# Optimization experiments

Hardware: AMD Instinct MI355X
Metric: run time of the kernel (lower is better)

The kernel has to match this reference:

```python
import jax, jax.numpy as jnp
import numpy as np

B, S, E, F = 8, 1024, 1024, 4096
EPS = 1e-12

def _layer_norm(x, gamma, beta):
    mu = jnp.mean(x, axis=-1, keepdims=True)
    var = jnp.mean(jnp.square(x - mu), axis=-1, keepdims=True)
    return (x - mu) / jnp.sqrt(var + EPS) * gamma + beta

def setup_inputs() -> dict:
    key = jax.random.key(0)
    ks = jax.random.split(key, 16)
    sE = 1.0 / np.sqrt(E)
    sF = 1.0 / np.sqrt(F)
    return {
        'hidden_states': jax.random.normal(ks[0], (B, S, E), jnp.float32),
        'Wq': jax.random.normal(ks[1], (E, E), jnp.float32) * sE,
        'bq': jnp.zeros((E,), jnp.float32),
        'Wk': jax.random.normal(ks[2], (E, E), jnp.float32) * sE,
        'bk': jnp.zeros((E,), jnp.float32),
        'Wv': jax.random.normal(ks[3], (E, E), jnp.float32) * sE,
        'bv': jnp.zeros((E,), jnp.float32),
        'Wd': jax.random.normal(ks[4], (E, E), jnp.float32) * sE,
        'bd': jnp.zeros((E,), jnp.float32),
        'g1': jnp.ones((E,), jnp.float32),
        'b1': jnp.zeros((E,), jnp.float32),
        'Wi': jax.random.normal(ks[5], (E, F), jnp.float32) * sE,
        'bi': jnp.zeros((F,), jnp.float32),
        'Wo': jax.random.normal(ks[6], (F, E), jnp.float32) * sF,
        'bo': jnp.zeros((E,), jnp.float32),
        'g2': jnp.ones((E,), jnp.float32),
        'b2': jnp.zeros((E,), jnp.float32),
    }

def reference(hidden_states, Wq, bq, Wk, bk, Wv, bv, Wd, bd, g1, b1, Wi, bi, Wo, bo, g2, b2):
    x = hidden_states
    q = x @ Wq + bq                     # [B,S,E]
    k = x @ Wk + bk
    v = x @ Wv + bv
    scores = jnp.einsum('bqe,bke->bqk', q, k) / jnp.sqrt(jnp.float32(E))
    attn_w = jax.nn.softmax(scores, axis=-1)
    attn_out = jnp.einsum('bqk,bke->bqe', attn_w, v)
    # add_norm 1 (dropout = identity in eval)
    h1 = _layer_norm(attn_out @ Wd + bd + x, g1, b1)
    ff = jax.nn.gelu(h1 @ Wi + bi, approximate=False)   # forward_act
    # NOTE: original code's second add_norm uses forward_act (pre out_dense),
    # applying out_dense inside add_norm -> LN(out_dense(ff) + h1)
    out = _layer_norm(ff @ Wo + bo + h1, g2, b2)
    return out
```

## Files before the change

### kernel.cpp

```cpp
#include <hip/hip_runtime.h>
#include <math.h>


typedef __bf16 bf16;
typedef __attribute__((ext_vector_type(8))) __bf16 bf16x8;
typedef __attribute__((ext_vector_type(4))) __bf16 bf16x4;
typedef __attribute__((ext_vector_type(4))) float f32x4;

#define BM 128
#define BN 128
#define BK 64
#define SCS 140

__device__ __forceinline__ void async_cp16(const bf16* g, bf16* l) {
    __builtin_amdgcn_global_load_lds((__attribute__((address_space(1))) void*)(g),
                                     (__attribute__((address_space(3))) void*)(l),
                                     16, 0, 0);
}

__device__ __forceinline__ float gelu_fast(float x) {
    float u = x * x;
    float y = 1.5957691216f * x * fmaf(0.044715f, u, 1.0f);
    float e = __expf(-y);
    return x * __builtin_amdgcn_rcpf(1.0f + e);
}

__device__ __forceinline__ float load_dual(const void* p, long long i, int f32) {
    return f32 ? ((const float*)p)[i] : (float)((const bf16*)p)[i];
}


__global__ void diag_init(const void* x, int* dflag)
{
    const int t = threadIdx.x;
    const bf16* xb = (const bf16*)x;
    float a = (float)xb[2 * t];
    float b = (float)xb[2 * t + 1];
    auto wild = [](float v) -> bool {
        float af = fabsf(v);
        return !(af <= 3.0e38f) || af > 1.0e3f || (v != 0.0f && af < 1.0e-8f);
    };
    unsigned long long ba = __ballot(wild(a));
    unsigned long long bb = __ballot(wild(b));
    if (t == 0) *dflag = (__popcll(ba) + __popcll(bb) > 16) ? 1 : 0;
}

__global__ void sentinel_small(float* out) { out[0] = 2048.0f; }


__global__ __launch_bounds__(256)
void convert_vec4(const void* src, bf16* dst, long long n4, const int* dflag)
{
    const int f32 = *dflag;
    long long i = (long long)blockIdx.x * 256 + threadIdx.x;
    if (i >= n4) return;
    bf16x4 o;
    if (f32) {
        f32x4 v = ((const f32x4*)src)[i];
        #pragma unroll
        for (int j = 0; j < 4; j++) o[j] = (bf16)v[j];
    } else {
        o = ((const bf16x4*)src)[i];
    }
    ((bf16x4*)dst)[i] = o;
}

struct SmallPtrs { const void* p[10]; };

__global__ __launch_bounds__(256)
void convert_small(SmallPtrs sp, bf16* dst, const int* dflag)
{
    const int f32 = *dflag;
    const int idx = blockIdx.x * 256 + threadIdx.x;
    if (idx >= 13312) return;
    const int seg = idx >> 10;
    float v;
    if (seg < 9) v = load_dual(sp.p[seg], idx & 1023, f32);
    else         v = load_dual(sp.p[9], idx - 9216, f32);
    dst[idx] = (bf16)v;
}

__global__ __launch_bounds__(256)
void transpose_dual(const void* in, bf16* out, int R, int C, const int* dflag)
{
    __shared__ bf16 tile[32][33];
    const int f32 = *dflag;
    const int c0 = blockIdx.x * 32, r0 = blockIdx.y * 32;
    const int tx = threadIdx.x, ty = threadIdx.y;
    #pragma unroll
    for (int i = 0; i < 32; i += 8)
        tile[ty + i][tx] = (bf16)load_dual(in, (long long)(r0 + ty + i) * C + (c0 + tx), f32);
    __syncthreads();
    #pragma unroll
    for (int i = 0; i < 32; i += 8)
        out[(long long)(c0 + ty + i) * R + (r0 + tx)] = tile[tx][ty + i];
}

__global__ __launch_bounds__(256)
void transpose_b(const bf16* __restrict__ in, bf16* __restrict__ out, int R, int C)
{
    __shared__ bf16 tile[32][33];
    const long long z = (long long)blockIdx.z * (long long)R * C;
    const int c0 = blockIdx.x * 32, r0 = blockIdx.y * 32;
    const int tx = threadIdx.x, ty = threadIdx.y;
    #pragma unroll
    for (int i = 0; i < 32; i += 8)
        tile[ty + i][tx] = in[z + (long long)(r0 + ty + i) * C + (c0 + tx)];
    __syncthreads();
    #pragma unroll
    for (int i = 0; i < 32; i += 8)
        out[z + (long long)(c0 + ty + i) * R + (r0 + tx)] = tile[tx][ty + i];
}

template<int ACT, int HAS_BIAS, int HAS_RES, int OUT_F32>
__global__ __launch_bounds__(512)
void gemm_bt(const bf16* __restrict__ A, const bf16* __restrict__ Bt,
             const bf16* __restrict__ bias, const bf16* __restrict__ res,
             void* __restrict__ Cout, int M, int N, int K, float scale,
             long long bsA, long long bsB, long long bsC, long long bsBias)
{
    __shared__ __align__(16) char smem[65536];
    float* sC = (float*)smem;

    const int tid  = threadIdx.x;
    const int lane = tid & 63;
    const int wave = tid >> 6;
    const int pw   = wave & 3;
    const int wm   = pw >> 1;
    const int wn   = pw & 1;
    const bool producer = (wave >= 4);
    const int m0   = blockIdx.y * BM;
    const int n0   = blockIdx.x * BN;
    const long long zA = (long long)blockIdx.z * bsA;
    const long long zB = (long long)blockIdx.z * bsB;
    const long long zC = (long long)blockIdx.z * bsC;
    const bf16* biasz = HAS_BIAS ? (bias + (long long)blockIdx.z * bsBias) : nullptr;
    const int nIter = K >> 6;

    f32x4 acc[4][4];
    const bf16* gA[4]; const bf16* gB[4]; int lo[4];

    if (producer) {
        #pragma unroll
        for (int j = 0; j < 4; j++) {
            const int ci  = j * 256 + pw * 64 + lane;
            const int row = ci >> 3;
            const int c8  = ((ci & 7) ^ (row & 7)) * 8;
            gA[j] = A + zA + (long long)(m0 + row) * K + c8;
            gB[j] = Bt + zB + (long long)(n0 + row) * K + c8;
            lo[j] = (j * 256 + pw * 64) * 8;
        }
        bf16* dA = (bf16*)smem;
        bf16* dB = (bf16*)(smem + 16384);
        #pragma unroll
        for (int j = 0; j < 4; j++) {
            async_cp16(gA[j], dA + lo[j]);
            async_cp16(gB[j], dB + lo[j]);
            gA[j] += BK; gB[j] += BK;
        }
    } else {
        const f32x4 zf = {0.f, 0.f, 0.f, 0.f};
        #pragma unroll
        for (int i = 0; i < 4; i++)
            #pragma unroll
            for (int j = 0; j < 4; j++) acc[i][j] = zf;
    }
    __syncthreads();

    const int fr   = lane & 15;
    const int x0   = (lane >> 4) ^ (fr & 7);
    const int arow = wm * 64 + fr;
    const int brow = wn * 64 + fr;

    for (int kt = 0; kt < nIter; ++kt) {
        if (producer) {
            if (kt + 1 < nIter) {
                const int bo = ((kt + 1) & 1) ? 32768 : 0;
                bf16* dA = (bf16*)(smem + bo);
                bf16* dB = (bf16*)(smem + bo + 16384);
                #pragma unroll
                for (int j = 0; j < 4; j++) {
                    async_cp16(gA[j], dA + lo[j]);
                    async_cp16(gB[j], dB + lo[j]);
                    gA[j] += BK; gB[j] += BK;
                }
            }
        } else {
            const int bo = (kt & 1) ? 32768 : 0;
            const bf16* sAk = (const bf16*)(smem + bo);
            const bf16* sBk = (const bf16*)(smem + bo + 16384);
            #pragma unroll
            for (int s = 0; s < 2; s++) {
                const int xo = (x0 ^ (s << 2)) * 8;
                bf16x8 afr[4], bfr[4];
                #pragma unroll
                for (int mi = 0; mi < 4; mi++) afr[mi] = *(const bf16x8*)(sAk + (arow + mi * 16) * 64 + xo);
                #pragma unroll
                for (int ni = 0; ni < 4; ni++) bfr[ni] = *(const bf16x8*)(sBk + (brow + ni * 16) * 64 + xo);
                #pragma unroll
                for (int mi = 0; mi < 4; mi++)
                    #pragma unroll
                    for (int ni = 0; ni < 4; ni++)
                        acc[mi][ni] = __builtin_amdgcn_mfma_f32_16x16x32_bf16(afr[mi], bfr[ni], acc[mi][ni], 0, 0, 0);
            }
        }
        __syncthreads();
    }

    const int q4 = lane >> 4;
    for (int h = 0; h < 2; h++) {
        __syncthreads();
        if (!producer && wm == h) {
            #pragma unroll
            for (int mi = 0; mi < 4; mi++)
                #pragma unroll
                for (int r = 0; r < 4; r++) {
                    const int lr = mi * 16 + q4 * 4 + r;
                    #pragma unroll
                    for (int ni = 0; ni < 4; ni++)
                        sC[lr * SCS + wn * 64 + ni * 16 + fr] = acc[mi][ni][r];
                }
        }
        __syncthreads();
        const int lr = tid >> 3;
        const int cb = (tid & 7) * 16;
        const long long grow  = m0 + h * 64 + lr;
        const long long gbase = zC + grow * (long long)N + (n0 + cb);
        const float* srow = sC + lr * SCS + cb;
        #pragma unroll
        for (int g = 0; g < 2; g++) {
            f32x4 v0 = *(const f32x4*)(srow + g * 8);
            f32x4 v1 = *(const f32x4*)(srow + g * 8 + 4);
            float vv[8] = {v0[0], v0[1], v0[2], v0[3], v1[0], v1[1], v1[2], v1[3]};
            if constexpr (HAS_BIAS) {
                bf16x8 bb = *(const bf16x8*)(biasz + n0 + cb + g * 8);
                #pragma unroll
                for (int j = 0; j < 8; j++) vv[j] = vv[j] * scale + (float)bb[j];
            } else {
                #pragma unroll
                for (int j = 0; j < 8; j++) vv[j] *= scale;
            }
            if constexpr (ACT == 1) {
                #pragma unroll
                for (int j = 0; j < 8; j++) vv[j] = gelu_fast(vv[j]);
            }
            if constexpr (HAS_RES) {
                bf16x8 rr = *(const bf16x8*)(res + gbase + g * 8);
                #pragma unroll
                for (int j = 0; j < 8; j++) vv[j] += (float)rr[j];
            }
            if constexpr (OUT_F32) {
                f32x4 o0 = {vv[0], vv[1], vv[2], vv[3]};
                f32x4 o1 = {vv[4], vv[5], vv[6], vv[7]};
                *(f32x4*)((float*)Cout + gbase + g * 8)     = o0;
                *(f32x4*)((float*)Cout + gbase + g * 8 + 4) = o1;
            } else {
                bf16x8 o;
                #pragma unroll
                for (int j = 0; j < 8; j++) o[j] = (bf16)vv[j];
                *(bf16x8*)((bf16*)Cout + gbase + g * 8) = o;
            }
        }
    }
}

template<int ACT, int HAS_BIAS, int HAS_RES, int OUT_F32, int SPLITK>
__global__ __launch_bounds__(512, 2)
void gemm256(const bf16* __restrict__ A, const bf16* __restrict__ Bt,
             const bf16* __restrict__ bias, const bf16* __restrict__ res,
             void* __restrict__ Cout, void* __restrict__ Cout2,
             int M, int N, int K, int ldk, float scale,
             long long bsB, long long bsC, long long bsBias)
{
    __shared__ __align__(16) char smem[131072];

    const int tid  = threadIdx.x;
    const int lane = tid & 63;
    const int wave = tid >> 6;
    const int wm   = wave >> 2;
    const int wn   = wave & 3;

    const int gx  = N >> 8;
    const int nwg = gx * (M >> 8);
    int wg = blockIdx.x;
    {
        const int q = nwg >> 3, r = nwg & 7;
        const int xcd = wg & 7, lid = wg >> 3;
        wg = (xcd < r ? xcd * (q + 1) : r * (q + 1) + (xcd - r) * q) + lid;
    }
    const int bx = wg % gx, by = wg / gx;
    const int m0 = by << 8, n0 = bx << 8;
    const int zi = blockIdx.y;

    const bf16* Ab = A  + (SPLITK ? (long long)zi * K : 0);
    const bf16* Bb = Bt + (SPLITK ? (long long)zi * K : (long long)zi * bsB);
    const bool  bon = HAS_BIAS && (!SPLITK || zi == 0);
    const bool  ron = HAS_RES  && (!SPLITK || zi == 0);
    const bf16* biasz = HAS_BIAS ? (bias + (SPLITK ? 0 : (long long)zi * bsBias)) : nullptr;
    const long long coff = SPLITK ? 0 : (long long)zi * bsC;
    char* const Cb = (char*)((SPLITK && zi) ? Cout2 : Cout);

    const int rg0 = wave * 16 + (lane >> 3);
    const int cg0 = (lane & 7) ^ (lane >> 3);
    const bf16* aSrc[2]; const bf16* bSrc[2];
    #pragma unroll
    for (int h = 0; h < 2; h++) {
        aSrc[h] = Ab + (long long)(m0 + h * 128 + rg0) * ldk + cg0 * 8;
        bSrc[h] = Bb + (long long)(n0 + h * 128 + rg0) * ldk + cg0 * 8;
    }
    const int sq8 = 8 * ldk;

    const int fr = lane & 15, chk = lane >> 4;
    unsigned aAddr[4], bAddr[4];
    {
        const unsigned sm3 = (unsigned)(size_t)(__attribute__((address_space(3))) char*)smem;
        #pragma unroll
        for (int cb = 0; cb < 2; cb++)
            #pragma unroll
            for (int kk = 0; kk < 2; kk++) {
                const unsigned slot = (unsigned)(((kk * 4 + chk) ^ (fr & 7)) * 16);
                aAddr[cb * 2 + kk] = sm3 + cb * 65536 + wm * 16384
                                   + fr * 128 + slot;
                bAddr[cb * 2 + kk] = sm3 + cb * 65536 + 32768 + (wn >> 1) * 16384
                                   + ((wn & 1) * 64 + fr) * 128 + slot;
            }
    }

#define DSR(d, b, imm) \
    asm volatile("ds_read_b128 %0, %1 offset:%c2" : "=v"(d) : "v"(b), "i"(imm))
#define RDA4(set, cb, q) do { \
    DSR(set[0], aAddr[(cb) * 2 + 0], (q) * 4096); \
    DSR(set[1], aAddr[(cb) * 2 + 1], (q) * 4096); \
    DSR(set[2], aAddr[(cb) * 2 + 0], (q) * 4096 + 2048); \
    DSR(set[3], aAddr[(cb) * 2 + 1], (q) * 4096 + 2048); \
} while (0)
#define RDB8(cb) do { \
    DSR(bv[0], bAddr[(cb) * 2 + 0], 0);    DSR(bv[1], bAddr[(cb) * 2 + 1], 0); \
    DSR(bv[2], bAddr[(cb) * 2 + 0], 2048); DSR(bv[3], bAddr[(cb) * 2 + 1], 2048); \
    DSR(bv[4], bAddr[(cb) * 2 + 0], 4096); DSR(bv[5], bAddr[(cb) * 2 + 1], 4096); \
    DSR(bv[6], bAddr[(cb) * 2 + 0], 6144); DSR(bv[7], bAddr[(cb) * 2 + 1], 6144); \
} while (0)
#define STG(buf, mat, h, t) do { \
    bf16* _d = (bf16*)(smem + (buf) * 65536 + (mat) * 32768 + (h) * 16384 + wave * 2048); \
    const bf16* _s = ((mat) ? bSrc[h] : aSrc[h]) + (t) * 64; \
    async_cp16(_s, _d); \
    async_cp16(_s + sq8, _d + 512); \
} while (0)
#define IF_STG(c, buf, mat, h, t) do { if (c) STG(buf, mat, h, t); } while (0)
#define BARR __builtin_amdgcn_s_barrier()
#define SB0  __builtin_amdgcn_sched_barrier(0)
#define LGKM0 asm volatile("s_waitcnt lgkmcnt(0)")
#define VM_WAIT(c) do { \
    if (c) asm volatile("s_waitcnt vmcnt(4)"); \
    else   asm volatile("s_waitcnt vmcnt(0)"); \
} while (0)
#define MMA(q, ASET) do { \
    __builtin_amdgcn_s_setprio(1); \
    _Pragma("unroll") \
    for (int _j = 0; _j < 4; _j++) { \
        acc[(q) * 2 + 0][_j] = __builtin_amdgcn_mfma_f32_16x16x32_bf16(ASET[0], bv[_j * 2 + 0], acc[(q) * 2 + 0][_j], 0, 0, 0); \
        acc[(q) * 2 + 1][_j] = __builtin_amdgcn_mfma_f32_16x16x32_bf16(ASET[2], bv[_j * 2 + 0], acc[(q) * 2 + 1][_j], 0, 0, 0); \
    } \
    _Pragma("unroll") \
    for (int _j = 0; _j < 4; _j++) { \
        acc[(q) * 2 + 0][_j] = __builtin_amdgcn_mfma_f32_16x16x32_bf16(ASET[1], bv[_j * 2 + 1], acc[(q) * 2 + 0][_j], 0, 0, 0); \
        acc[(q) * 2 + 1][_j] = __builtin_amdgcn_mfma_f32_16x16x32_bf16(ASET[3], bv[_j * 2 + 1], acc[(q) * 2 + 1][_j], 0, 0, 0); \
    } \
    __builtin_amdgcn_s_setprio(0); \
} while (0)

    const int NT = K >> 6, NI = NT >> 1;

    STG(0, 0, 0, 0); STG(0, 0, 1, 0); STG(0, 1, 0, 0); STG(0, 1, 1, 0);
    STG(1, 1, 0, 1); STG(1, 1, 1, 1);

    f32x4 acc[8][4];
    {
        const f32x4 zf = {0.f, 0.f, 0.f, 0.f};
        #pragma unroll
        for (int i = 0; i < 8; i++)
            #pragma unroll
            for (int j = 0; j < 4; j++) acc[i][j] = zf;
    }
    bf16x8 avA[4], avB[4], bv[8];

    asm volatile("s_waitcnt vmcnt(4)");
    BARR;

    for (int it = 0; it < NI; ++it) {
        const int o = 2 * it + 1, e2 = 2 * it + 2, o2 = 2 * it + 3;
        const bool se = e2 < NT, so = o2 < NT;
        RDB8(0);
        RDA4(avA, 0, 0);
        STG(1, 0, 0, o);
        BARR; LGKM0; SB0;
        RDA4(avB, 0, 1); SB0;
        MMA(0, avA);
        BARR;
        STG(1, 0, 1, o);
        BARR; LGKM0; SB0;
        RDA4(avA, 0, 2); SB0;
        MMA(1, avB);
        BARR;
        IF_STG(se, 0, 1, 0, e2);
        BARR; LGKM0; SB0;
        RDA4(avB, 0, 3); SB0;
        MMA(2, avA);
        BARR;
        IF_STG(se, 0, 1, 1, e2);
        BARR; LGKM0; SB0;
        MMA(3, avB); SB0;
        VM_WAIT(se);
        BARR;
        RDB8(1);
        RDA4(avA, 1, 0);
        IF_STG(se, 0, 0, 0, e2);
        BARR; LGKM0; SB0;
        RDA4(avB, 1, 1); SB0;
        MMA(0, avA);
        BARR;
        IF_STG(se, 0, 0, 1, e2);
        BARR; LGKM0; SB0;
        RDA4(avA, 1, 2); SB0;
        MMA(1, avB);
        BARR;
        IF_STG(so, 1, 1, 0, o2);
        BARR; LGKM0; SB0;
        RDA4(avB, 1, 3); SB0;
        MMA(2, avA);
        BARR;
        IF_STG(so, 1, 1, 1, o2);
        BARR; LGKM0; SB0;
        MMA(3, avB); SB0;
        VM_WAIT(so);
        BARR;
    }
#undef MMA
#undef VM_WAIT
#undef LGKM0
#undef SB0
#undef BARR
#undef IF_STG
#undef STG
#undef RDB8
#undef RDA4
#undef DSR

    float* sC = (float*)smem;
    const int q4 = lane >> 4;
    const int lr = tid >> 3;
    const int c0 = (tid & 7) * 4;
    const long long Nll = N;
    #pragma unroll
    for (int p = 0; p < 4; p++) {
        __syncthreads();
        if (wm == (p >> 1)) {
            #pragma unroll
            for (int i = 0; i < 4; i++) {
                const int fi = (p & 1) * 4 + i;
                #pragma unroll
                for (int r = 0; r < 4; r++) {
                    const int row = i * 16 + q4 * 4 + r;
                    #pragma unroll
                    for (int j = 0; j < 4; j++)
                        sC[row * 260 + wn * 64 + j * 16 + fr] = acc[fi][j][r];
                }
            }
        }
        __syncthreads();
        const long long grow = m0 + p * 64 + lr;
        const long long gb = grow * Nll + n0;
        const float* srow = sC + lr * 260;
        #pragma unroll
        for (int g = 0; g < 8; g++) {
            const int col = c0 + g * 32;
            f32x4 v = *(const f32x4*)(srow + col);
            float vv[4] = {v[0], v[1], v[2], v[3]};
            if (bon) {
                bf16x4 bb = *(const bf16x4*)(biasz + n0 + col);
                #pragma unroll
                for (int j = 0; j < 4; j++) vv[j] = vv[j] * scale + (float)bb[j];
            } else {
                #pragma unroll
                for (int j = 0; j < 4; j++) vv[j] *= scale;
            }
            if constexpr (ACT == 1) {
                #pragma unroll
                for (int j = 0; j < 4; j++) vv[j] = gelu_fast(vv[j]);
            }
            if (ron) {
                bf16x4 rr = *(const bf16x4*)(res + gb + col);
                #pragma unroll
                for (int j = 0; j < 4; j++) vv[j] += (float)rr[j];
            }
            if constexpr (OUT_F32) {
                f32x4 o4 = {vv[0], vv[1], vv[2], vv[3]};
                *(f32x4*)((float*)Cb + coff + gb + col) = o4;
            } else {
                bf16x4 o4;
                #pragma unroll
                for (int j = 0; j < 4; j++) o4[j] = (bf16)vv[j];
                *(bf16x4*)((bf16*)Cb + coff + gb + col) = o4;
            }
        }
    }
}

template<int ACT, int HAS_BIAS, int HAS_RES, int OUT_F32, int SPLITK>
__global__ __launch_bounds__(512, 4)
void gemm128d(const bf16* __restrict__ A, const bf16* __restrict__ Bt,
              const bf16* __restrict__ bias, const bf16* __restrict__ res,
              void* __restrict__ Cout, void* __restrict__ Cout2,
              int M, int N, int K, int ldk, float scale,
              long long bsA, long long bsB, long long bsC, long long bsBias)
{
    __shared__ __align__(16) char smem[65536];

    const int tid  = threadIdx.x;
    const int lane = tid & 63;
    const int wave = tid >> 6;
    const int wm   = wave >> 2;
    const int wn   = wave & 3;

    const int gx  = N >> 7;
    const int nwg = gx * (M >> 7);
    int wg = blockIdx.x;
    {
        const int q = nwg >> 3, r = nwg & 7;
        const int xcd = wg & 7, lid = wg >> 3;
        wg = (xcd < r ? xcd * (q + 1) : r * (q + 1) + (xcd - r) * q) + lid;
    }
    const int bx = wg % gx, by = wg / gx;
    const int m0 = by << 7, n0 = bx << 7;
    const int zi = blockIdx.y;

    const bf16* Ab = A  + (SPLITK ? (long long)zi * K : (long long)zi * bsA);
    const bf16* Bb = Bt + (SPLITK ? (long long)zi * K : (long long)zi * bsB);
    const bool  bon = HAS_BIAS && (!SPLITK || zi == 0);
    const bool  ron = HAS_RES  && (!SPLITK || zi == 0);
    const bf16* biasz = HAS_BIAS ? (bias + (SPLITK ? 0 : (long long)zi * bsBias)) : nullptr;
    const long long coff = SPLITK ? 0 : (long long)zi * bsC;
    char* const Cb = (char*)((SPLITK && zi) ? Cout2 : Cout);

    const int rg0 = wave * 16 + (lane >> 3);
    const int cg0 = (lane & 7) ^ (lane >> 3);
    const bf16* aSrc = Ab + (long long)(m0 + rg0) * ldk + cg0 * 8;
    const bf16* bSrc = Bb + (long long)(n0 + rg0) * ldk + cg0 * 8;
    const int sq8 = 8 * ldk;

    const int fr = lane & 15, chk = lane >> 4;
    unsigned aAd[2][2], bAd[2][2];
    {
        const unsigned sm3 = (unsigned)(size_t)(__attribute__((address_space(3))) char*)smem;
        #pragma unroll
        for (int p = 0; p < 2; p++)
            #pragma unroll
            for (int kk = 0; kk < 2; kk++) {
                const unsigned slot = (unsigned)(((kk * 4 + chk) ^ (fr & 7)) * 16);
                aAd[p][kk] = sm3 + p * 32768 + (wm * 64 + fr) * 128 + slot;
                bAd[p][kk] = sm3 + p * 32768 + 16384 + (wn * 32 + fr) * 128 + slot;
            }
    }

#define DSR(d, b, imm) \
    asm volatile("ds_read_b128 %0, %1 offset:%c2" : "=v"(d) : "v"(b), "i"(imm))
#define MM8(mh) do { \
    _Pragma("unroll") \
    for (int _n = 0; _n < 2; _n++) { \
        acc[(mh) * 2 + 0][_n] = __builtin_amdgcn_mfma_f32_16x16x32_bf16(av[((mh) * 2 + 0) * 2 + 0], bv[_n * 2 + 0], acc[(mh) * 2 + 0][_n], 0, 0, 0); \
        acc[(mh) * 2 + 1][_n] = __builtin_amdgcn_mfma_f32_16x16x32_bf16(av[((mh) * 2 + 1) * 2 + 0], bv[_n * 2 + 0], acc[(mh) * 2 + 1][_n], 0, 0, 0); \
    } \
    _Pragma("unroll") \
    for (int _n = 0; _n < 2; _n++) { \
        acc[(mh) * 2 + 0][_n] = __builtin_amdgcn_mfma_f32_16x16x32_bf16(av[((mh) * 2 + 0) * 2 + 1], bv[_n * 2 + 1], acc[(mh) * 2 + 0][_n], 0, 0, 0); \
        acc[(mh) * 2 + 1][_n] = __builtin_amdgcn_mfma_f32_16x16x32_bf16(av[((mh) * 2 + 1) * 2 + 1], bv[_n * 2 + 1], acc[(mh) * 2 + 1][_n], 0, 0, 0); \
    } \
} while (0)
#define TILE(p, SC) do { \
    DSR(bv[0], bAd[p][0], 0);    DSR(bv[1], bAd[p][1], 0); \
    DSR(bv[2], bAd[p][0], 2048); DSR(bv[3], bAd[p][1], 2048); \
    DSR(av[0], aAd[p][0], 0);    DSR(av[1], aAd[p][1], 0); \
    DSR(av[2], aAd[p][0], 2048); DSR(av[3], aAd[p][1], 2048); \
    DSR(av[4], aAd[p][0], 4096); DSR(av[5], aAd[p][1], 4096); \
    DSR(av[6], aAd[p][0], 6144); DSR(av[7], aAd[p][1], 6144); \
    if (SC) { \
        bf16* _dA = (bf16*)(smem + ((p) ^ 1) * 32768 + wave * 2048); \
        bf16* _dB = (bf16*)(smem + ((p) ^ 1) * 32768 + 16384 + wave * 2048); \
        async_cp16(aSrc, _dA);       async_cp16(aSrc + sq8, _dA + 512); \
        async_cp16(bSrc, _dB);       async_cp16(bSrc + sq8, _dB + 512); \
        aSrc += 64; bSrc += 64; \
    } \
    asm volatile("s_waitcnt lgkmcnt(4)"); \
    __builtin_amdgcn_sched_barrier(0); \
    __builtin_amdgcn_s_setprio(1); \
    MM8(0); \
    __builtin_amdgcn_s_setprio(0); \
    asm volatile("s_waitcnt lgkmcnt(0)"); \
    __builtin_amdgcn_sched_barrier(0); \
    __builtin_amdgcn_s_setprio(1); \
    MM8(1); \
    __builtin_amdgcn_s_setprio(0); \
    __builtin_amdgcn_sched_barrier(0); \
    asm volatile("s_waitcnt vmcnt(0)"); \
    __builtin_amdgcn_s_barrier(); \
} while (0)

    const int NT = K >> 6, NH = NT >> 1;

    {
        bf16* dA = (bf16*)(smem + wave * 2048);
        bf16* dB = (bf16*)(smem + 16384 + wave * 2048);
        async_cp16(aSrc, dA);       async_cp16(aSrc + sq8, dA + 512);
        async_cp16(bSrc, dB);       async_cp16(bSrc + sq8, dB + 512);
        aSrc += 64; bSrc += 64;
    }

    f32x4 acc[4][2];
    {
        const f32x4 zf = {0.f, 0.f, 0.f, 0.f};
        #pragma unroll
        for (int i = 0; i < 4; i++) {
            acc[i][0] = zf; acc[i][1] = zf;
        }
    }
    bf16x8 av[8], bv[4];

    asm volatile("s_waitcnt vmcnt(0)");
    __builtin_amdgcn_s_barrier();

    for (int it = 0; it < NH; ++it) {
        const bool so = (it + 1 < NH);
        TILE(0, true);
        TILE(1, so);
    }
#undef TILE
#undef MM8
#undef DSR

    float* sC = (float*)smem;
    const int q4 = lane >> 4;
    const int lr = tid >> 3;
    const int c0 = (tid & 7) * 4;
    const long long Nll = N;
    #pragma unroll
    for (int p2 = 0; p2 < 2; p2++) {
        __syncthreads();
        if (wm == p2) {
            #pragma unroll
            for (int mi = 0; mi < 4; mi++)
                #pragma unroll
                for (int r = 0; r < 4; r++) {
                    const int row = mi * 16 + q4 * 4 + r;
                    #pragma unroll
                    for (int ni = 0; ni < 2; ni++)
                        sC[row * 132 + wn * 32 + ni * 16 + fr] = acc[mi][ni][r];
                }
        }
        __syncthreads();
        const long long grow = m0 + p2 * 64 + lr;
        const long long gb = grow * Nll + n0;
        const float* srow = sC + lr * 132;
        #pragma unroll
        for (int g = 0; g < 4; g++) {
            const int col = c0 + g * 32;
            f32x4 v = *(const f32x4*)(srow + col);
            float vv[4] = {v[0], v[1], v[2], v[3]};
            if (bon) {
                bf16x4 bb = *(const bf16x4*)(biasz + n0 + col);
                #pragma unroll
                for (int j = 0; j < 4; j++) vv[j] = vv[j] * scale + (float)bb[j];
            } else {
                #pragma unroll
                for (int j = 0; j < 4; j++) vv[j] *= scale;
            }
            if constexpr (ACT == 1) {
                #pragma unroll
                for (int j = 0; j < 4; j++) vv[j] = gelu_fast(vv[j]);
            }
            if (ron) {
                bf16x4 rr = *(const bf16x4*)(res + gb + col);
                #pragma unroll
                for (int j = 0; j < 4; j++) vv[j] += (float)rr[j];
            }
            if constexpr (OUT_F32) {
                f32x4 o4 = {vv[0], vv[1], vv[2], vv[3]};
                *(f32x4*)((float*)Cb + coff + gb + col) = o4;
            } else {
                bf16x4 o4;
                #pragma unroll
                for (int j = 0; j < 4; j++) o4[j] = (bf16)vv[j];
                *(bf16x4*)((bf16*)Cb + coff + gb + col) = o4;
            }
        }
    }
}


__global__ __launch_bounds__(256)
void softmax_inplace(bf16* __restrict__ P, int N)
{
    const long long row = blockIdx.x;
    bf16* p = P + row * (long long)N;
    const int t = threadIdx.x;
    bf16x4 xin = *(const bf16x4*)(p + t * 4);
    float xs[4];
    #pragma unroll
    for (int i = 0; i < 4; i++) xs[i] = (float)xin[i];

    float m = fmaxf(fmaxf(xs[0], xs[1]), fmaxf(xs[2], xs[3]));
    #pragma unroll
    for (int off = 32; off > 0; off >>= 1) m = fmaxf(m, __shfl_xor(m, off, 64));
    __shared__ float red[4];
    if ((t & 63) == 0) red[t >> 6] = m;
    __syncthreads();
    m = fmaxf(fmaxf(red[0], red[1]), fmaxf(red[2], red[3]));

    float e[4], s = 0.f;
    #pragma unroll
    for (int i = 0; i < 4; i++) { e[i] = __expf(xs[i] - m); s += e[i]; }
    #pragma unroll
    for (int off = 32; off > 0; off >>= 1) s += __shfl_xor(s, off, 64);
    __shared__ float red2[4];
    if ((t & 63) == 0) red2[t >> 6] = s;
    __syncthreads();
    s = red2[0] + red2[1] + red2[2] + red2[3];
    const float inv = 1.f / s;

    bf16x4 o;
    #pragma unroll
    for (int i = 0; i < 4; i++) o[i] = (bf16)(e[i] * inv);
    *(bf16x4*)(p + t * 4) = o;
}

template<int IN_MODE, int OUT_F32>
__global__ __launch_bounds__(256)
void layernorm_rows(const void* __restrict__ Z, const void* __restrict__ Z2,
                    const bf16* __restrict__ g, const bf16* __restrict__ b,
                    void* __restrict__ outp, int N)
{
    const long long row = blockIdx.x;
    const int t = threadIdx.x;
    float xv[4];
    if constexpr (IN_MODE >= 1) {
        f32x4 zin = *(const f32x4*)((const float*)Z + row * (long long)N + t * 4);
        #pragma unroll
        for (int i = 0; i < 4; i++) xv[i] = zin[i];
        if constexpr (IN_MODE == 2) {
            f32x4 z2 = *(const f32x4*)((const float*)Z2 + row * (long long)N + t * 4);
            #pragma unroll
            for (int i = 0; i < 4; i++) xv[i] += z2[i];
        }
    } else {
        bf16x4 zin = *(const bf16x4*)((const bf16*)Z + row * (long long)N + t * 4);
        #pragma unroll
        for (int i = 0; i < 4; i++) xv[i] = (float)zin[i];
    }

    float s = xv[0] + xv[1] + xv[2] + xv[3];
    #pragma unroll
    for (int off = 32; off > 0; off >>= 1) s += __shfl_xor(s, off, 64);
    __shared__ float r1[4];
    if ((t & 63) == 0) r1[t >> 6] = s;
    __syncthreads();
    const float mu = (r1[0] + r1[1] + r1[2] + r1[3]) * (1.f / 1024.f);

    float d[4];
    float sq = 0.f;
    #pragma unroll
    for (int i = 0; i < 4; i++) { d[i] = xv[i] - mu; sq += d[i] * d[i]; }
    #pragma unroll
    for (int off = 32; off > 0; off >>= 1) sq += __shfl_xor(sq, off, 64);
    __shared__ float r2[4];
    if ((t & 63) == 0) r2[t >> 6] = sq;
    __syncthreads();
    const float var = (r2[0] + r2[1] + r2[2] + r2[3]) * (1.f / 1024.f);
    const float rstd = rsqrtf(var + 1e-12f);

    bf16x4 gv = *(const bf16x4*)(g + t * 4);
    bf16x4 bv = *(const bf16x4*)(b + t * 4);
    if constexpr (OUT_F32) {
        f32x4 o;
        #pragma unroll
        for (int i = 0; i < 4; i++)
            o[i] = d[i] * rstd * (float)gv[i] + (float)bv[i];
        *(f32x4*)((float*)outp + row * (long long)N + t * 4) = o;
    } else {
        bf16x4 o;
        #pragma unroll
        for (int i = 0; i < 4; i++)
            o[i] = (bf16)(d[i] * rstd * (float)gv[i] + (float)bv[i]);
        *(bf16x4*)((bf16*)outp + row * (long long)N + t * 4) = o;
    }
}


extern "C" void kernel_launch(void* const* d_in, const int* in_sizes, int n_in,
                              void* d_out, int out_size, void* d_ws, size_t ws_size,
                              hipStream_t stream)
{
    (void)in_sizes; (void)n_in; (void)out_size;

    const void* x  = d_in[0];
    const void* Wq = d_in[1];  const void* bq = d_in[2];
    const void* Wk = d_in[3];  const void* bk = d_in[4];
    const void* Wv = d_in[5];  const void* bv = d_in[6];
    const void* Wd = d_in[7];  const void* bd = d_in[8];
    const void* g1 = d_in[9];  const void* b1 = d_in[10];
    const void* Wi = d_in[11]; const void* bi = d_in[12];
    const void* Wo = d_in[13]; const void* bo = d_in[14];
    const void* g2 = d_in[15]; const void* b2 = d_in[16];

    const int Bb = 8, S = 1024, E = 1024, F = 4096;
    const int M = Bb * S;
    const long long SE = (long long)S * E, SS = (long long)S * S;
    const long long ME = (long long)M * E;

    char* ws = (char*)d_ws;
    const size_t MB = 1024ull * 1024ull;
    int*  dflag = (int*)(ws + 0);
    bf16* small = (bf16*)(ws + 64 * 1024);
    bf16* bq_c = small + 0 * 1024;
    bf16* bd_c = small + 3 * 1024;
    bf16* g1_c = small + 4 * 1024;
    bf16* b1_c = small + 5 * 1024;
    bf16* g2_c = small + 6 * 1024;
    bf16* b2_c = small + 7 * 1024;
    bf16* bo_c = small + 8 * 1024;
    bf16* bi_c = small + 9216;
    bf16* WoT  = (bf16*)(ws + 1 * MB);
    bf16* WiT  = (bf16*)(ws + 9 * MB);
    bf16* WqT  = (bf16*)(ws + 17 * MB);
    bf16* WkT  = (bf16*)(ws + 19 * MB);
    bf16* WvT  = (bf16*)(ws + 21 * MB);
    bf16* WdT  = (bf16*)(ws + 23 * MB);
    bf16* xb   = (bf16*)(ws + 25 * MB);
    float* out = (float*)d_out;

    diag_init<<<1, 64, 0, stream>>>(x, dflag);

    if (ws_size < 70 * MB) { sentinel_small<<<1, 1, 0, stream>>>(out); return; }

    SmallPtrs sp;
    sp.p[0] = bq; sp.p[1] = bk; sp.p[2] = bv; sp.p[3] = bd; sp.p[4] = g1;
    sp.p[5] = b1; sp.p[6] = g2; sp.p[7] = b2; sp.p[8] = bo; sp.p[9] = bi;
    convert_small<<<52, 256, 0, stream>>>(sp, small, dflag);
    convert_vec4<<<8192, 256, 0, stream>>>(x, xb, ME / 4, dflag);

    const dim3 tb(32, 8, 1);
    transpose_dual<<<dim3(E/32, E/32), tb, 0, stream>>>(Wq, WqT, E, E, dflag);
    transpose_dual<<<dim3(E/32, E/32), tb, 0, stream>>>(Wk, WkT, E, E, dflag);
    transpose_dual<<<dim3(E/32, E/32), tb, 0, stream>>>(Wv, WvT, E, E, dflag);
    transpose_dual<<<dim3(E/32, E/32), tb, 0, stream>>>(Wd, WdT, E, E, dflag);
    transpose_dual<<<dim3(F/32, E/32), tb, 0, stream>>>(Wi, WiT, E, F, dflag);
    transpose_dual<<<dim3(E/32, F/32), tb, 0, stream>>>(Wo, WoT, F, E, dflag);

    if (ws_size >= 121 * MB) {
        bf16* qkv  = (bf16*)(ws + 41 * MB);
        bf16* q    = qkv;
        bf16* k    = qkv + ME;
        bf16* v    = qkv + 2 * ME;
        bf16* vT   = (bf16*)(ws + 89 * MB);
        bf16* P    = (bf16*)(ws + 73 * MB);
        bf16* attn = (bf16*)(ws + 41 * MB);
        bf16* z1   = (bf16*)(ws + 57 * MB);
        bf16* h1   = (bf16*)(ws + 41 * MB);
        bf16* ff   = (bf16*)(ws + 57 * MB);
        float* z2f = (float*)(ws + 9 * MB);

        gemm256<0,1,0,0,0><<<dim3((E/256)*(M/256), 3), 512, 0, stream>>>(
            xb, WqT, bq_c, nullptr, qkv, nullptr, M, E, E, E, 1.f,
            (long long)E * E, ME, E);
        transpose_b<<<dim3(E/32, S/32, Bb), tb, 0, stream>>>(v, vT, S, E);
        gemm128d<0,0,0,0,0><<<dim3((S/128)*(S/128), Bb), 512, 0, stream>>>(
            q, k, nullptr, nullptr, P, nullptr, S, S, E, E, 0.03125f,
            SE, SE, SS, 0);
        softmax_inplace<<<M, 256, 0, stream>>>(P, S);
        gemm128d<0,0,0,0,0><<<dim3((E/128)*(S/128), Bb), 512, 0, stream>>>(
            P, vT, nullptr, nullptr, attn, nullptr, S, E, S, S, 1.f,
            SS, SE, SE, 0);
        gemm128d<0,1,1,0,0><<<dim3((E/128)*(M/128), 1), 512, 0, stream>>>(
            attn, WdT, bd_c, xb, z1, nullptr, M, E, E, E, 1.f, 0, 0, 0, 0);
        layernorm_rows<0,0><<<M, 256, 0, stream>>>(z1, nullptr, g1_c, b1_c, h1, E);
        gemm256<1,1,0,0,0><<<dim3((F/256)*(M/256), 1), 512, 0, stream>>>(
            h1, WiT, bi_c, nullptr, ff, nullptr, M, F, E, E, 1.f, 0, 0, 0);
        gemm128d<0,1,1,1,0><<<dim3((E/128)*(M/128), 1), 512, 0, stream>>>(
            ff, WoT, bo_c, h1, z2f, nullptr, M, E, F, F, 1.f, 0, 0, 0, 0);
        layernorm_rows<1,1><<<M, 256, 0, stream>>>(z2f, nullptr, g2_c, b2_c, out, E);
    } else {
        bf16* qkv_b = (bf16*)(ws + 41 * MB);
        bf16* q_b   = qkv_b;
        bf16* k_b   = qkv_b + SE;
        bf16* v_b   = qkv_b + 2 * SE;
        bf16* vT_b  = (bf16*)(ws + 47 * MB);
        bf16* P_b   = (bf16*)(ws + 49 * MB);
        bf16* at_b  = (bf16*)(ws + 51 * MB);
        bf16* z1_b  = (bf16*)(ws + 53 * MB);
        bf16* h1_b  = (bf16*)(ws + 55 * MB);
        bf16* ff_b  = (bf16*)(ws + 57 * MB);
        bf16* z2_b  = (bf16*)(ws + 65 * MB);

        for (int b = 0; b < Bb; b++) {
            const bf16* x_b = xb + (long long)b * SE;
            gemm_bt<0,1,0,0><<<dim3(8, 8, 3), 512, 0, stream>>>(
                x_b, WqT, bq_c, nullptr, qkv_b, S, E, E, 1.f, 0, (long long)E * E, SE, E);
            transpose_b<<<dim3(E/32, S/32), tb, 0, stream>>>(v_b, vT_b, S, E);
            gemm_bt<0,0,0,0><<<dim3(8, 8), 512, 0, stream>>>(
                q_b, k_b, nullptr, nullptr, P_b, S, S, E, 0.03125f, 0, 0, 0, 0);
            softmax_inplace<<<S, 256, 0, stream>>>(P_b, S);
            gemm_bt<0,0,0,0><<<dim3(8, 8), 512, 0, stream>>>(
                P_b, vT_b, nullptr, nullptr, at_b, S, E, S, 1.f, 0, 0, 0, 0);
            gemm_bt<0,1,1,0><<<dim3(8, 8), 512, 0, stream>>>(
                at_b, WdT, bd_c, x_b, z1_b, S, E, E, 1.f, 0, 0, 0, 0);
            layernorm_rows<0,0><<<S, 256, 0, stream>>>(z1_b, nullptr, g1_c, b1_c, h1_b, E);
            gemm_bt<1,1,0,0><<<dim3(32, 8), 512, 0, stream>>>(
                h1_b, WiT, bi_c, nullptr, ff_b, S, F, E, 1.f, 0, 0, 0, 0);
            gemm_bt<0,1,1,0><<<dim3(8, 8), 512, 0, stream>>>(
                ff_b, WoT, bo_c, h1_b, z2_b, S, E, F, 1.f, 0, 0, 0, 0);
            layernorm_rows<0,1><<<S, 256, 0, stream>>>(z2_b, nullptr, g2_c, b2_c, out + (long long)b * SE, E);
        }
    }
}
```

Measured before the change: 481.0 us.

## Split-K the FFN output GEMM into two bf16 partials and batch weight transposes

```diff
diff --git a/kernel.cpp b/kernel.cpp
--- a/kernel.cpp
+++ b/kernel.cpp
@@ -85,6 +85,26 @@
 {
     __shared__ bf16 tile[32][33];
     const int f32 = *dflag;
+    const int c0 = blockIdx.x * 32, r0 = blockIdx.y * 32;
+    const int tx = threadIdx.x, ty = threadIdx.y;
+    #pragma unroll
+    for (int i = 0; i < 32; i += 8)
+        tile[ty + i][tx] = (bf16)load_dual(in, (long long)(r0 + ty + i) * C + (c0 + tx), f32);
+    __syncthreads();
+    #pragma unroll
+    for (int i = 0; i < 32; i += 8)
+        out[(long long)(c0 + ty + i) * R + (r0 + tx)] = tile[tx][ty + i];
+}
+
+struct W4Ptrs { const void* p[4]; };
+
+__global__ __launch_bounds__(256)
+void transpose_quad(W4Ptrs wp, bf16* outbase, int R, int C, const int* dflag)
+{
+    __shared__ bf16 tile[32][33];
+    const int f32 = *dflag;
+    const void* in = wp.p[blockIdx.z];
+    bf16* out = outbase + (long long)blockIdx.z * (long long)R * C;
     const int c0 = blockIdx.x * 32, r0 = blockIdx.y * 32;
     const int tx = threadIdx.x, ty = threadIdx.y;
     #pragma unroll
@@ -741,7 +761,7 @@
     const long long row = blockIdx.x;
     const int t = threadIdx.x;
     float xv[4];
-    if constexpr (IN_MODE >= 1) {
+    if constexpr (IN_MODE == 1 || IN_MODE == 2) {
         f32x4 zin = *(const f32x4*)((const float*)Z + row * (long long)N + t * 4);
         #pragma unroll
         for (int i = 0; i < 4; i++) xv[i] = zin[i];
@@ -754,6 +774,11 @@
         bf16x4 zin = *(const bf16x4*)((const bf16*)Z + row * (long long)N + t * 4);
         #pragma unroll
         for (int i = 0; i < 4; i++) xv[i] = (float)zin[i];
+        if constexpr (IN_MODE == 3) {
+            bf16x4 z2 = *(const bf16x4*)((const bf16*)Z2 + row * (long long)N + t * 4);
+            #pragma unroll
+            for (int i = 0; i < 4; i++) xv[i] += (float)z2[i];
+        }
     }
 
     float s = xv[0] + xv[1] + xv[2] + xv[3];
@@ -847,10 +872,8 @@
     convert_vec4<<<8192, 256, 0, stream>>>(x, xb, ME / 4, dflag);
 
     const dim3 tb(32, 8, 1);
-    transpose_dual<<<dim3(E/32, E/32), tb, 0, stream>>>(Wq, WqT, E, E, dflag);
-    transpose_dual<<<dim3(E/32, E/32), tb, 0, stream>>>(Wk, WkT, E, E, dflag);
-    transpose_dual<<<dim3(E/32, E/32), tb, 0, stream>>>(Wv, WvT, E, E, dflag);
-    transpose_dual<<<dim3(E/32, E/32), tb, 0, stream>>>(Wd, WdT, E, E, dflag);
+    W4Ptrs wp; wp.p[0] = Wq; wp.p[1] = Wk; wp.p[2] = Wv; wp.p[3] = Wd;
+    transpose_quad<<<dim3(E/32, E/32, 4), tb, 0, stream>>>(wp, WqT, E, E, dflag);
     transpose_dual<<<dim3(F/32, E/32), tb, 0, stream>>>(Wi, WiT, E, F, dflag);
     transpose_dual<<<dim3(E/32, F/32), tb, 0, stream>>>(Wo, WoT, F, E, dflag);
 
@@ -865,7 +888,8 @@
         bf16* z1   = (bf16*)(ws + 57 * MB);
         bf16* h1   = (bf16*)(ws + 41 * MB);
         bf16* ff   = (bf16*)(ws + 57 * MB);
-        float* z2f = (float*)(ws + 9 * MB);
+        bf16* z2a  = (bf16*)(ws + 9 * MB);
+        bf16* z2b  = (bf16*)(ws + 25 * MB);
 
         gemm256<0,1,0,0,0><<<dim3((E/256)*(M/256), 3), 512, 0, stream>>>(
             xb, WqT, bq_c, nullptr, qkv, nullptr, M, E, E, E, 1.f,
@@ -883,9 +907,9 @@
         layernorm_rows<0,0><<<M, 256, 0, stream>>>(z1, nullptr, g1_c, b1_c, h1, E);
         gemm256<1,1,0,0,0><<<dim3((F/256)*(M/256), 1), 512, 0, stream>>>(
             h1, WiT, bi_c, nullptr, ff, nullptr, M, F, E, E, 1.f, 0, 0, 0);
-        gemm128d<0,1,1,1,0><<<dim3((E/128)*(M/128), 1), 512, 0, stream>>>(
-            ff, WoT, bo_c, h1, z2f, nullptr, M, E, F, F, 1.f, 0, 0, 0, 0);
-        layernorm_rows<1,1><<<M, 256, 0, stream>>>(z2f, nullptr, g2_c, b2_c, out, E);
+        gemm256<0,1,1,0,1><<<dim3((E/256)*(M/256), 2), 512, 0, stream>>>(
+            ff, WoT, bo_c, h1, z2a, z2b, M, E, F / 2, F, 1.f, 0, 0, 0);
+        layernorm_rows<3,1><<<M, 256, 0, stream>>>(z2a, z2b, g2_c, b2_c, out, E);
     } else {
         bf16* qkv_b = (bf16*)(ws + 41 * MB);
         bf16* q_b   = qkv_b;
```

After: 482.5 us. No clear change (+0.3%).
